# Kernel optimization log

Hardware: AMD Instinct MI355X
Metric: run time of the kernel (lower is better)

Reference implementation:

```python
import jax, jax.numpy as jnp
import numpy as np

B, F, T, C = 128, 512, 60, 15  # batch, feature_size, timesteps, num_cameras
H1, H2 = 128, 64               # decoder hidden channels


def setup_inputs() -> dict:
    key = jax.random.key(0)
    ks = jax.random.split(key, 6)
    x = jax.random.normal(ks[0], (B, F, T), dtype=jnp.float32)
    cam = jax.random.randint(ks[1], (B,), 0, C)
    # per-camera (expert) decoder params
    W1 = jax.random.normal(ks[2], (C, F, H1, 3, 4), dtype=jnp.float32) * 0.02  # ConvT3d F->128, k=(1,3,4)
    b1 = jnp.zeros((C, H1), dtype=jnp.float32)
    W2 = jax.random.normal(ks[3], (C, H1, H2, 3, 4), dtype=jnp.float32) * 0.02  # ConvT3d 128->64, k=s=(1,3,4)
    b2 = jnp.zeros((C, H2), dtype=jnp.float32)
    W3 = jax.random.normal(ks[4], (C, H2), dtype=jnp.float32) * 0.02            # Conv3d 64->1, k=1
    b3 = jnp.zeros((C,), dtype=jnp.float32)
    return {"x": x, "cam": cam, "W1": W1, "b1": b1, "W2": W2, "b2": b2, "W3": W3, "b3": b3}


def reference(x, cam, W1, b1, W2, b2, W3, b3):
    # MoE-style dispatch: gather each sample's camera-expert weights.
    # Layer 1: transposed conv from 1x1 -> 3x4 is a pure linear map over features.
    h1 = jnp.einsum('bft,bfopq->btopq', x, W1[cam]) + b1[cam][:, None, :, None, None]
    h1 = jax.nn.relu(h1)                                # (B,T,128,3,4)
    # Layer 2: stride == kernel => non-overlapping transposed conv, out[3p+r,4q+s].
    h2 = jnp.einsum('btipq,biors->btoprqs', h1, W2[cam])  # (B,T,64,3,3,4,4)
    h2 = h2.reshape(B, T, H2, 9, 16) + b2[cam][:, None, :, None, None]
    h2 = jax.nn.relu(h2)                                # (B,T,64,9,16)
    # Layer 3: 1x1x1 conv to a single channel, then squeeze + sigmoid.
    out = jnp.einsum('btohw,bo->bthw', h2, W3[cam]) + b3[cam][:, None, None, None]
    return jax.nn.sigmoid(out)                           # (B,T,9,16)
```

## Files before the change

kernel.cpp:

```cpp
#include <hip/hip_runtime.h>
#include <hip/hip_bf16.h>
#include <cstdint>

#define B_  128
#define F_  512
#define T_  60
#define C_  15
#define H1_ 128
#define H2_ 64

typedef short short8_t __attribute__((ext_vector_type(8)));
typedef float f32x4    __attribute__((ext_vector_type(4)));

static __device__ __forceinline__ unsigned short f2bf(float f) {
    union { float f; uint32_t u; } v; v.f = f;
    uint32_t r = v.u + 0x7FFF + ((v.u >> 16) & 1);
    return (unsigned short)(r >> 16);
}

static __device__ __forceinline__ void async_cp16(const unsigned short* g, unsigned short* l) {
    __builtin_amdgcn_global_load_lds(
        (const __attribute__((address_space(1))) unsigned int*)g,
        (__attribute__((address_space(3))) unsigned int*)l, 16, 0, 0);
}

__global__ __launch_bounds__(256) void prep_all(
    const float* __restrict__ x, const float* __restrict__ W2,
    const float* __restrict__ W1, const int* __restrict__ cam,
    unsigned short* __restrict__ xTs, unsigned short* __restrict__ W2f,
    unsigned short* __restrict__ W1s, int* __restrict__ ord)
{
    __shared__ float sm[12288];
    const int blk = blockIdx.x, tid = threadIdx.x;

    if (blk < 512) {
        float (*xs)[61] = (float(*)[61])sm;
        const int f0 = (blk & 3) * 128, b = blk >> 2;
        #pragma unroll
        for (int it = 0; it < 32; ++it) {
            int idx = tid + it * 256;
            int fl = idx >> 6, t = idx & 63;
            if (t < T_) xs[fl][t] = x[((size_t)b * F_ + f0 + fl) * T_ + t];
        }
        __syncthreads();
        #pragma unroll
        for (int it = 0; it < 8; ++it) {
            int idx = tid + it * 256;
            int t = idx >> 5, f4 = (idx & 31) * 4;
            ushort4 o;
            o.x = (t < T_) ? f2bf(xs[f4 + 0][t]) : 0;
            o.y = (t < T_) ? f2bf(xs[f4 + 1][t]) : 0;
            o.z = (t < T_) ? f2bf(xs[f4 + 2][t]) : 0;
            o.w = (t < T_) ? f2bf(xs[f4 + 3][t]) : 0;
            const int f = f0 + f4;
            const int kc = f >> 6, within = f & 63;
            const int cc = (within >> 3) ^ (t & 7), half = (within >> 2) & 1;
            *(ushort4*)(xTs + (size_t)b * 32768 + kc * 4096 + t * 64 + cc * 8 + half * 4) = o;
        }
    } else if (blk < 632) {
        float (*ls)[384] = (float(*)[384])sm;
        const int id = blk - 512;
        const int i0 = (id & 3) * 32, o0 = ((id >> 2) & 1) * 32, c = id >> 3;
        #pragma unroll
        for (int it = 0; it < 12; ++it) {
            int idx = tid + it * 256;
            int il = idx / 96, r = idx - il * 96;
            float4 v = *(const float4*)(W2 + ((size_t)(c * H1_ + i0 + il)) * (H2_ * 12)
                                           + (size_t)o0 * 12 + r * 4);
            *(float4*)&ls[il][r * 4] = v;
        }
        __syncthreads();
        const int o_l = tid >> 3, i_l = (tid & 7) * 4;
        const int o  = o0 + o_l;
        const int nt = o >> 4, l15 = o & 15;
        const int lane = l15 + 16 * ((i_l >> 3) & 3);
        const int kk  = i0 >> 5;
        const int pos = i_l & 7;
        #pragma unroll
        for (int rs = 0; rs < 12; ++rs) {
            ushort4 v;
            v.x = f2bf(ls[i_l + 0][o_l * 12 + rs]);
            v.y = f2bf(ls[i_l + 1][o_l * 12 + rs]);
            v.z = f2bf(ls[i_l + 2][o_l * 12 + rs]);
            v.w = f2bf(ls[i_l + 3][o_l * 12 + rs]);
            *(ushort4*)(W2f + ((size_t)(c * 12 + rs) * 16 + nt * 4 + kk) * 512
                            + lane * 8 + pos) = v;
        }
    } else if (blk == 632) {
        int* cs = (int*)sm;
        if (tid < B_) cs[tid] = cam[tid];
        __syncthreads();
        if (tid < B_) {
            const int cb = cs[tid];
            int rank = 0;
            #pragma unroll 16
            for (int j = 0; j < B_; ++j) {
                int cj = cs[j];
                rank += (cj < cb || (cj == cb && j < tid)) ? 1 : 0;
            }
            ord[rank] = tid;
        }
    } else {
        float (*ls)[384] = (float(*)[384])sm;
        const int id = blk - 633;
        const int f0 = (id & 15) * 32, i0 = ((id >> 4) & 3) * 32, c = id >> 6;
        #pragma unroll
        for (int it = 0; it < 12; ++it) {
            int idx = tid + it * 256;
            int fl = idx / 96, r = idx - fl * 96;
            float4 v = *(const float4*)(W1 + ((size_t)(c * F_ + f0 + fl)) * (H1_ * 12)
                                           + (size_t)i0 * 12 + r * 4);
            *(float4*)&ls[fl][r * 4] = v;
        }
        __syncthreads();
        const int i_l = tid >> 3, f_l = (tid & 7) * 4;
        const int i = i0 + i_l, f = f0 + f_l;
        const int kc = f >> 6, within = f & 63;
        const int cc = (within >> 3) ^ (i & 7), half = (within >> 2) & 1;
        #pragma unroll
        for (int pq = 0; pq < 12; ++pq) {
            ushort4 o;
            o.x = f2bf(ls[f_l + 0][i_l * 12 + pq]);
            o.y = f2bf(ls[f_l + 1][i_l * 12 + pq]);
            o.z = f2bf(ls[f_l + 2][i_l * 12 + pq]);
            o.w = f2bf(ls[f_l + 3][i_l * 12 + pq]);
            *(ushort4*)(W1s + (size_t)(c * 12 + pq) * 65536
                            + kc * 8192 + i * 64 + cc * 8 + half * 4) = o;
        }
    }
}

__global__ __launch_bounds__(256) void fused_all(
    const unsigned short* __restrict__ xTs, const unsigned short* __restrict__ W1s,
    const unsigned short* __restrict__ W2f, const int* __restrict__ cam,
    const int* __restrict__ ord,
    const float* __restrict__ b1, const float* __restrict__ b2,
    const float* __restrict__ W3, const float* __restrict__ b3,
    float* __restrict__ out)
{
    __shared__ __align__(16) unsigned short smem[24576];

    const int idx = blockIdx.x;
    const int swz = (idx & 7) * 192 + (idx >> 3);
    const int bpos = swz / 12, pq = swz - bpos * 12;
    const int b = ord[bpos];

    const int tid = threadIdx.x;
    const int w = tid >> 6, l = tid & 63;
    const int l15 = l & 15, g = l >> 4;
    const int c = cam[b];

    const unsigned short* xchunk = xTs + (size_t)b * 32768;
    const unsigned short* wchunk = W1s + (size_t)(c * 12 + pq) * 65536;

    #define STAGE1(kc, buf)                                                       \
        {                                                                         \
            _Pragma("unroll")                                                     \
            for (int k = 0; k < 2; ++k)                                           \
                async_cp16(xchunk + (kc) * 4096 + (w * 2 + k) * 512 + l * 8,      \
                           smem + (buf) * 12288 + (w * 2 + k) * 512 + l * 8);     \
            _Pragma("unroll")                                                     \
            for (int k = 0; k < 4; ++k)                                           \
                async_cp16(wchunk + (kc) * 8192 + (w * 4 + k) * 512 + l * 8,      \
                           smem + (buf) * 12288 + 4096 + (w * 4 + k) * 512 + l * 8); \
        }

    f32x4 acc1[4][2];
    #pragma unroll
    for (int mt = 0; mt < 4; ++mt) {
        acc1[mt][0] = (f32x4){0.f, 0.f, 0.f, 0.f};
        acc1[mt][1] = (f32x4){0.f, 0.f, 0.f, 0.f};
    }

    STAGE1(0, 0);
    STAGE1(1, 1);

    const int sxor = (l15 & 7);
    #pragma unroll
    for (int kc = 0; kc < 8; ++kc) {
        if (kc < 7) { asm volatile("s_waitcnt vmcnt(6)" ::: "memory"); }
        else        { asm volatile("s_waitcnt vmcnt(0)" ::: "memory"); }
        __builtin_amdgcn_s_barrier();
        asm volatile("" ::: "memory");

        const int base = (kc & 1) * 12288;
        #pragma unroll
        for (int kk2 = 0; kk2 < 2; ++kk2) {
            const int cc = (kk2 * 4 + g) ^ sxor;
            short8_t af[4], bf[2];
            #pragma unroll
            for (int mt = 0; mt < 4; ++mt)
                af[mt] = *(const short8_t*)(smem + base + (16 * mt + l15) * 64 + cc * 8);
            #pragma unroll
            for (int ni = 0; ni < 2; ++ni)
                bf[ni] = *(const short8_t*)(smem + base + 4096
                                            + (32 * w + 16 * ni + l15) * 64 + cc * 8);
            #pragma unroll
            for (int mt = 0; mt < 4; ++mt)
                #pragma unroll
                for (int ni = 0; ni < 2; ++ni)
                    acc1[mt][ni] = __builtin_amdgcn_mfma_f32_16x16x32_bf16(
                        af[mt], bf[ni], acc1[mt][ni], 0, 0, 0);
        }

        asm volatile("" ::: "memory");
        __builtin_amdgcn_s_barrier();
        if (kc < 6) STAGE1(kc + 2, kc & 1);
    }
    #undef STAGE1

    const unsigned short* W2base = W2f + (size_t)(c * 12 + w * 3) * 8192;
    short8_t bfr[2][4];
    #pragma unroll
    for (int kk = 0; kk < 4; ++kk)
        bfr[0][kk] = *(const short8_t*)(W2base + kk * 512 + l * 8);

    float w3v[4][4], b2v[4][4];
    #pragma unroll
    for (int nt = 0; nt < 4; ++nt)
        #pragma unroll
        for (int r = 0; r < 4; ++r) {
            w3v[nt][r] = W3[c * H2_ + nt * 16 + g * 4 + r];
            b2v[nt][r] = b2[c * H2_ + nt * 16 + g * 4 + r];
        }
    const float b3v = b3[c];
    const int p = pq >> 2, q = pq & 3;

    unsigned short* h1s = smem;
    #pragma unroll
    for (int ni = 0; ni < 2; ++ni) {
        const int i = 32 * w + 16 * ni + l15;
        const float b1v = b1[c * H1_ + i];
        #pragma unroll
        for (int mt = 0; mt < 4; ++mt)
            #pragma unroll
            for (int r = 0; r < 4; ++r) {
                float h = acc1[mt][ni][r] + b1v;
                h = h > 0.f ? h : 0.f;
                h1s[(16 * mt + 4 * g + r) * 136 + i] = f2bf(h);
            }
    }
    __syncthreads();

    short8_t a2[4][4];
    #pragma unroll
    for (int mt = 0; mt < 4; ++mt)
        #pragma unroll
        for (int kk = 0; kk < 4; ++kk)
            a2[mt][kk] = *(const short8_t*)&h1s[(16 * mt + l15) * 136 + 32 * kk + 8 * g];

    float s[4] = {0.f, 0.f, 0.f, 0.f};

    #pragma unroll
    for (int seg = 0; seg < 12; ++seg) {
        if (seg < 11) {
            const int ns = seg + 1;
            const unsigned short* nb = W2base + (ns >> 2) * 8192 + ((ns & 3) * 4) * 512;
            #pragma unroll
            for (int kk = 0; kk < 4; ++kk)
                bfr[(seg + 1) & 1][kk] = *(const short8_t*)(nb + kk * 512 + l * 8);
        }
        const int nt = seg & 3;
        #pragma unroll
        for (int mt = 0; mt < 4; ++mt) {
            f32x4 acc2 = (f32x4){0.f, 0.f, 0.f, 0.f};
            #pragma unroll
            for (int kk = 0; kk < 4; ++kk)
                acc2 = __builtin_amdgcn_mfma_f32_16x16x32_bf16(
                    bfr[seg & 1][kk], a2[mt][kk], acc2, 0, 0, 0);
            #pragma unroll
            for (int r = 0; r < 4; ++r)
                s[mt] = fmaf(w3v[nt][r], fmaxf(acc2[r] + b2v[nt][r], 0.f), s[mt]);
        }

        if (nt == 3) {
            const int rs = w * 3 + (seg >> 2);
            const int hrow = p * 3 + (rs >> 2), wcol = q * 4 + (rs & 3);
            #pragma unroll
            for (int mt = 0; mt < 4; ++mt) {
                s[mt] += __shfl_xor(s[mt], 16);
                s[mt] += __shfl_xor(s[mt], 32);
            }
            float v = (g & 1) ? ((g & 2) ? s[3] : s[1]) : ((g & 2) ? s[2] : s[0]);
            v += b3v;
            if (l < T_)
                out[(((size_t)b * T_ + l) * 9 + hrow) * 16 + wcol] =
                    1.f / (1.f + __expf(-v));
            s[0] = s[1] = s[2] = s[3] = 0.f;
        }
    }
}

__global__ __launch_bounds__(256) void fused_decoder_f32(
    const float* __restrict__ x,   const int* __restrict__ cam,
    const float* __restrict__ W1,  const float* __restrict__ b1,
    const float* __restrict__ W2,  const float* __restrict__ b2,
    const float* __restrict__ W3,  const float* __restrict__ b3,
    float* __restrict__ out)
{
    __shared__ float h1s[T_ * H1_];
    __shared__ float stage[8192];

    const int pq  = blockIdx.x;
    const int b   = blockIdx.y;
    const int p   = pq >> 2, q = pq & 3;
    const int tid = threadIdx.x;
    const int c   = cam[b];

    float* xs  = stage;
    float* w1s = stage + 2048;

    const int ig = tid & 31;
    const int tg = tid >> 5;

    float acc[8][4];
    #pragma unroll
    for (int a = 0; a < 8; ++a)
        #pragma unroll
        for (int j = 0; j < 4; ++j) acc[a][j] = 0.f;

    for (int f0 = 0; f0 < F_; f0 += 32) {
        __syncthreads();
        {
            int lane = tid & 63;
            int sub  = tid >> 6;
            if (lane < T_) {
                #pragma unroll
                for (int m = 0; m < 8; ++m) {
                    int kk = sub * 8 + m;
                    xs[kk * 64 + lane] = x[((size_t)b * F_ + f0 + kk) * T_ + lane];
                }
            }
        }
        for (int e = tid; e < 32 * H1_; e += 256) {
            int kk = e >> 7, i = e & 127;
            w1s[e] = W1[(((size_t)c * F_ + f0 + kk) * H1_ + i) * 12 + pq];
        }
        __syncthreads();
        #pragma unroll 8
        for (int kk = 0; kk < 32; ++kk) {
            float4 bv = *(const float4*)&w1s[kk * 128 + ig * 4];
            float4 a0 = *(const float4*)&xs[kk * 64 + tg * 8];
            float4 a1 = *(const float4*)&xs[kk * 64 + tg * 8 + 4];
            float at[8] = {a0.x, a0.y, a0.z, a0.w, a1.x, a1.y, a1.z, a1.w};
            #pragma unroll
            for (int tt = 0; tt < 8; ++tt) {
                acc[tt][0] = fmaf(at[tt], bv.x, acc[tt][0]);
                acc[tt][1] = fmaf(at[tt], bv.y, acc[tt][1]);
                acc[tt][2] = fmaf(at[tt], bv.z, acc[tt][2]);
                acc[tt][3] = fmaf(at[tt], bv.w, acc[tt][3]);
            }
        }
    }
    {
        float4 b1v = *(const float4*)&b1[c * H1_ + ig * 4];
        #pragma unroll
        for (int tt = 0; tt < 8; ++tt) {
            int t = tg * 8 + tt;
            if (t < T_) {
                float4 hv;
                hv.x = fmaxf(acc[tt][0] + b1v.x, 0.f);
                hv.y = fmaxf(acc[tt][1] + b1v.y, 0.f);
                hv.z = fmaxf(acc[tt][2] + b1v.z, 0.f);
                hv.w = fmaxf(acc[tt][3] + b1v.w, 0.f);
                *(float4*)&h1s[t * H1_ + ig * 4] = hv;
            }
        }
    }

    const int lane = tid & 63;
    const int wv   = tid >> 6;
    const float w3v = W3[c * H2_ + lane];
    const float b2v = b2[c * H2_ + lane];
    const float b3v = b3[c];
    float* w2s = stage;

    for (int rs = 0; rs < 12; ++rs) {
        __syncthreads();
        for (int e = tid; e < H1_ * H2_; e += 256) {
            int i = e >> 6, o = e & 63;
            w2s[e] = W2[(((size_t)c * H1_ + i) * H2_ + o) * 12 + rs];
        }
        __syncthreads();

        float acc2[15];
        #pragma unroll
        for (int j = 0; j < 15; ++j) acc2[j] = 0.f;

        for (int i = 0; i < H1_; i += 4) {
            float wa = w2s[(i + 0) * 64 + lane];
            float wb = w2s[(i + 1) * 64 + lane];
            float wc = w2s[(i + 2) * 64 + lane];
            float wd = w2s[(i + 3) * 64 + lane];
            #pragma unroll
            for (int j = 0; j < 15; ++j) {
                float4 h = *(const float4*)&h1s[(wv * 15 + j) * H1_ + i];
                acc2[j] = fmaf(h.x, wa, acc2[j]);
                acc2[j] = fmaf(h.y, wb, acc2[j]);
                acc2[j] = fmaf(h.z, wc, acc2[j]);
                acc2[j] = fmaf(h.w, wd, acc2[j]);
            }
        }

        const int r = rs >> 2, s = rs & 3;
        const int hrow = p * 3 + r, wcol = q * 4 + s;
        #pragma unroll
        for (int j = 0; j < 15; ++j) {
            float y = w3v * fmaxf(acc2[j] + b2v, 0.f);
            #pragma unroll
            for (int m = 32; m > 0; m >>= 1) y += __shfl_xor(y, m, 64);
            if (lane == j) {
                int t = wv * 15 + j;
                float v = y + b3v;
                out[(((size_t)b * T_ + t) * 9 + hrow) * 16 + wcol] = 1.f / (1.f + __expf(-v));
            }
        }
    }
}

extern "C" void kernel_launch(void* const* d_in, const int* in_sizes, int n_in,
                              void* d_out, int out_size, void* d_ws, size_t ws_size,
                              hipStream_t stream) {
    const float* x   = (const float*)d_in[0];
    const int*   cam = (const int*)  d_in[1];
    const float* W1  = (const float*)d_in[2];
    const float* b1  = (const float*)d_in[3];
    const float* W2  = (const float*)d_in[4];
    const float* b2  = (const float*)d_in[5];
    const float* W3  = (const float*)d_in[6];
    const float* b3  = (const float*)d_in[7];
    float* outp = (float*)d_out;

    const size_t n_xT  = (size_t)B_ * 32768;
    const size_t n_w1s = (size_t)C_ * 12 * 65536;
    const size_t n_w2f = (size_t)C_ * 12 * 16 * 512;
    const size_t needed = (n_xT + n_w1s + n_w2f) * sizeof(unsigned short)
                        + B_ * sizeof(int);

    if (d_ws != nullptr && ws_size >= needed) {
        unsigned short* xTs = (unsigned short*)d_ws;
        unsigned short* W1p = xTs + n_xT;
        unsigned short* W2p = W1p + n_w1s;
        int* ord = (int*)(W2p + n_w2f);
        prep_all<<<1593, 256, 0, stream>>>(x, W2, W1, cam, xTs, W2p, W1p, ord);
        fused_all<<<dim3(12 * B_), 256, 0, stream>>>(
            xTs, W1p, W2p, cam, ord, b1, b2, W3, b3, outp);
    } else {
        fused_decoder_f32<<<dim3(12, B_), 256, 0, stream>>>(
            x, cam, W1, b1, W2, b2, W3, b3, outp);
    }
}
```

Baseline: 60.58 us.

## Pair same-camera samples per block to share expert weight tiles

The prep kernel now groups samples with the same camera into chunks of up to two, and the fused kernel processes one chunk per block. The W1 expert tile is loaded once and used for two samples, doubling the M dimension of the first GEMM. Layer 2 runs once per sample and reuses the same W2 stream. This roughly halves W1 traffic and block count, at the cost of a larger LDS footprint (64KB), twice as many accumulator registers, fewer blocks, and duplicate work when a camera has an odd number of samples.

```diff
diff --git a/kernel.cpp b/kernel.cpp
--- a/kernel.cpp
+++ b/kernel.cpp
@@ -28,7 +28,8 @@
     const float* __restrict__ x, const float* __restrict__ W2,
     const float* __restrict__ W1, const int* __restrict__ cam,
     unsigned short* __restrict__ xTs, unsigned short* __restrict__ W2f,
-    unsigned short* __restrict__ W1s, int* __restrict__ ord)
+    unsigned short* __restrict__ W1s, int* __restrict__ chunks,
+    int* __restrict__ nchp)
 {
     __shared__ float sm[12288];
     const int blk = blockIdx.x, tid = threadIdx.x;
@@ -87,7 +88,8 @@
                             + lane * 8 + pos) = v;
         }
     } else if (blk == 632) {
-        int* cs = (int*)sm;
+        int* cs  = (int*)sm;
+        int* ods = cs + 128;
         if (tid < B_) cs[tid] = cam[tid];
         __syncthreads();
         if (tid < B_) {
@@ -98,7 +100,20 @@
                 int cj = cs[j];
                 rank += (cj < cb || (cj == cb && j < tid)) ? 1 : 0;
             }
-            ord[rank] = tid;
+            ods[rank] = tid;
+        }
+        __syncthreads();
+        if (tid == 0) {
+            int k = 0, j = 0;
+            while (j < B_) {
+                int b0 = ods[j], bn;
+                if (j + 1 < B_ && cs[ods[j + 1]] == cs[b0]) { bn = ods[j + 1]; j += 2; }
+                else { bn = b0; j += 1; }
+                chunks[2 * k]     = b0;
+                chunks[2 * k + 1] = bn;
+                ++k;
+            }
+            nchp[0] = k;
         }
     } else {
         float (*ls)[384] = (float(*)[384])sm;
@@ -133,41 +148,47 @@
 __global__ __launch_bounds__(256) void fused_all(
     const unsigned short* __restrict__ xTs, const unsigned short* __restrict__ W1s,
     const unsigned short* __restrict__ W2f, const int* __restrict__ cam,
-    const int* __restrict__ ord,
+    const int* __restrict__ chunks, const int* __restrict__ nchp,
     const float* __restrict__ b1, const float* __restrict__ b2,
     const float* __restrict__ W3, const float* __restrict__ b3,
     float* __restrict__ out)
 {
-    __shared__ __align__(16) unsigned short smem[24576];
+    __shared__ __align__(16) unsigned short smem[32768];
 
     const int idx = blockIdx.x;
-    const int swz = (idx & 7) * 192 + (idx >> 3);
-    const int bpos = swz / 12, pq = swz - bpos * 12;
-    const int b = ord[bpos];
+    const int swz = (idx & 7) * 108 + (idx >> 3);
+    const int chunk = swz / 12, pq = swz - chunk * 12;
+    if (chunk >= nchp[0]) return;
+    const int bA = chunks[2 * chunk], bB = chunks[2 * chunk + 1];
 
     const int tid = threadIdx.x;
     const int w = tid >> 6, l = tid & 63;
     const int l15 = l & 15, g = l >> 4;
-    const int c = cam[b];
-
-    const unsigned short* xchunk = xTs + (size_t)b * 32768;
+    const int c = cam[bA];
+
+    const unsigned short* xcA = xTs + (size_t)bA * 32768;
+    const unsigned short* xcB = xTs + (size_t)bB * 32768;
     const unsigned short* wchunk = W1s + (size_t)(c * 12 + pq) * 65536;
 
     #define STAGE1(kc, buf)                                                       \
         {                                                                         \
             _Pragma("unroll")                                                     \
             for (int k = 0; k < 2; ++k)                                           \
-                async_cp16(xchunk + (kc) * 4096 + (w * 2 + k) * 512 + l * 8,      \
-                           smem + (buf) * 12288 + (w * 2 + k) * 512 + l * 8);     \
+                async_cp16(xcA + (kc) * 4096 + (w * 2 + k) * 512 + l * 8,         \
+                           smem + (buf) * 16384 + (w * 2 + k) * 512 + l * 8);     \
+            _Pragma("unroll")                                                     \
+            for (int k = 0; k < 2; ++k)                                           \
+                async_cp16(xcB + (kc) * 4096 + (w * 2 + k) * 512 + l * 8,         \
+                           smem + (buf) * 16384 + 4096 + (w * 2 + k) * 512 + l * 8); \
             _Pragma("unroll")                                                     \
             for (int k = 0; k < 4; ++k)                                           \
                 async_cp16(wchunk + (kc) * 8192 + (w * 4 + k) * 512 + l * 8,      \
-                           smem + (buf) * 12288 + 4096 + (w * 4 + k) * 512 + l * 8); \
-        }
-
-    f32x4 acc1[4][2];
-    #pragma unroll
-    for (int mt = 0; mt < 4; ++mt) {
+                           smem + (buf) * 16384 + 8192 + (w * 4 + k) * 512 + l * 8); \
+        }
+
+    f32x4 acc1[8][2];
+    #pragma unroll
+    for (int mt = 0; mt < 8; ++mt) {
         acc1[mt][0] = (f32x4){0.f, 0.f, 0.f, 0.f};
         acc1[mt][1] = (f32x4){0.f, 0.f, 0.f, 0.f};
     }
@@ -178,25 +199,29 @@
     const int sxor = (l15 & 7);
     #pragma unroll
     for (int kc = 0; kc < 8; ++kc) {
-        if (kc < 7) { asm volatile("s_waitcnt vmcnt(6)" ::: "memory"); }
+        if (kc < 7) { asm volatile("s_waitcnt vmcnt(8)" ::: "memory"); }
         else        { asm volatile("s_waitcnt vmcnt(0)" ::: "memory"); }
         __builtin_amdgcn_s_barrier();
         asm volatile("" ::: "memory");
 
-        const int base = (kc & 1) * 12288;
+        const int base = (kc & 1) * 16384;
         #pragma unroll
         for (int kk2 = 0; kk2 < 2; ++kk2) {
             const int cc = (kk2 * 4 + g) ^ sxor;
-            short8_t af[4], bf[2];
+            short8_t af[8], bf[2];
             #pragma unroll
             for (int mt = 0; mt < 4; ++mt)
                 af[mt] = *(const short8_t*)(smem + base + (16 * mt + l15) * 64 + cc * 8);
             #pragma unroll
+            for (int mt = 0; mt < 4; ++mt)
+                af[4 + mt] = *(const short8_t*)(smem + base + 4096
+                                                + (16 * mt + l15) * 64 + cc * 8);
+            #pragma unroll
             for (int ni = 0; ni < 2; ++ni)
-                bf[ni] = *(const short8_t*)(smem + base + 4096
+                bf[ni] = *(const short8_t*)(smem + base + 8192
                                             + (32 * w + 16 * ni + l15) * 64 + cc * 8);
             #pragma unroll
-            for (int mt = 0; mt < 4; ++mt)
+            for (int mt = 0; mt < 8; ++mt)
                 #pragma unroll
                 for (int ni = 0; ni < 2; ++ni)
                     acc1[mt][ni] = __builtin_amdgcn_mfma_f32_16x16x32_bf16(
@@ -226,67 +251,81 @@
     const float b3v = b3[c];
     const int p = pq >> 2, q = pq & 3;
 
-    unsigned short* h1s = smem;
     #pragma unroll
     for (int ni = 0; ni < 2; ++ni) {
         const int i = 32 * w + 16 * ni + l15;
         const float b1v = b1[c * H1_ + i];
         #pragma unroll
-        for (int mt = 0; mt < 4; ++mt)
+        for (int mt = 0; mt < 8; ++mt) {
+            unsigned short* h1s = smem + (mt >> 2) * 16384;
+            const int mtl = mt & 3;
             #pragma unroll
             for (int r = 0; r < 4; ++r) {
                 float h = acc1[mt][ni][r] + b1v;
                 h = h > 0.f ? h : 0.f;
-                h1s[(16 * mt + 4 * g + r) * 136 + i] = f2bf(h);
-            }
+                h1s[(16 * mtl + 4 * g + r) * 136 + i] = f2bf(h);
+            }
+        }
     }
     __syncthreads();
 
-    short8_t a2[4][4];
-    #pragma unroll
-    for (int mt = 0; mt < 4; ++mt)
-        #pragma unroll
-        for (int kk = 0; kk < 4; ++kk)
-            a2[mt][kk] = *(const short8_t*)&h1s[(16 * mt + l15) * 136 + 32 * kk + 8 * g];
-
-    float s[4] = {0.f, 0.f, 0.f, 0.f};
-
-    #pragma unroll
-    for (int seg = 0; seg < 12; ++seg) {
-        if (seg < 11) {
-            const int ns = seg + 1;
-            const unsigned short* nb = W2base + (ns >> 2) * 8192 + ((ns & 3) * 4) * 512;
+    #pragma unroll
+    for (int smp = 0; smp < 2; ++smp) {
+        const unsigned short* h1s = smem + smp * 16384;
+        const int bb = smp ? bB : bA;
+
+        short8_t a2[4][4];
+        #pragma unroll
+        for (int mt = 0; mt < 4; ++mt)
             #pragma unroll
             for (int kk = 0; kk < 4; ++kk)
-                bfr[(seg + 1) & 1][kk] = *(const short8_t*)(nb + kk * 512 + l * 8);
-        }
-        const int nt = seg & 3;
-        #pragma unroll
-        for (int mt = 0; mt < 4; ++mt) {
-            f32x4 acc2 = (f32x4){0.f, 0.f, 0.f, 0.f};
+                a2[mt][kk] = *(const short8_t*)&h1s[(16 * mt + l15) * 136 + 32 * kk + 8 * g];
+
+        if (smp == 1) {
             #pragma unroll
             for (int kk = 0; kk < 4; ++kk)
-                acc2 = __builtin_amdgcn_mfma_f32_16x16x32_bf16(
-                    bfr[seg & 1][kk], a2[mt][kk], acc2, 0, 0, 0);
-            #pragma unroll
-            for (int r = 0; r < 4; ++r)
-                s[mt] = fmaf(w3v[nt][r], fmaxf(acc2[r] + b2v[nt][r], 0.f), s[mt]);
-        }
-
-        if (nt == 3) {
-            const int rs = w * 3 + (seg >> 2);
-            const int hrow = p * 3 + (rs >> 2), wcol = q * 4 + (rs & 3);
+                bfr[0][kk] = *(const short8_t*)(W2base + kk * 512 + l * 8);
+        }
+
+        float s[4] = {0.f, 0.f, 0.f, 0.f};
+
+        #pragma unroll
+        for (int seg = 0; seg < 12; ++seg) {
+            if (seg < 11) {
+                const int ns = seg + 1;
+                const unsigned short* nb = W2base + (ns >> 2) * 8192 + ((ns & 3) * 4) * 512;
+                #pragma unroll
+                for (int kk = 0; kk < 4; ++kk)
+                    bfr[(seg + 1) & 1][kk] = *(const short8_t*)(nb + kk * 512 + l * 8);
+            }
+            const int nt = seg & 3;
             #pragma unroll
             for (int mt = 0; mt < 4; ++mt) {
-                s[mt] += __shfl_xor(s[mt], 16);
-                s[mt] += __shfl_xor(s[mt], 32);
-            }
-            float v = (g & 1) ? ((g & 2) ? s[3] : s[1]) : ((g & 2) ? s[2] : s[0]);
-            v += b3v;
-            if (l < T_)
-                out[(((size_t)b * T_ + l) * 9 + hrow) * 16 + wcol] =
-                    1.f / (1.f + __expf(-v));
-            s[0] = s[1] = s[2] = s[3] = 0.f;
+                f32x4 acc2 = (f32x4){0.f, 0.f, 0.f, 0.f};
+                #pragma unroll
+                for (int kk = 0; kk < 4; ++kk)
+                    acc2 = __builtin_amdgcn_mfma_f32_16x16x32_bf16(
+                        bfr[seg & 1][kk], a2[mt][kk], acc2, 0, 0, 0);
+                #pragma unroll
+                for (int r = 0; r < 4; ++r)
+                    s[mt] = fmaf(w3v[nt][r], fmaxf(acc2[r] + b2v[nt][r], 0.f), s[mt]);
+            }
+
+            if (nt == 3) {
+                const int rs = w * 3 + (seg >> 2);
+                const int hrow = p * 3 + (rs >> 2), wcol = q * 4 + (rs & 3);
+                #pragma unroll
+                for (int mt = 0; mt < 4; ++mt) {
+                    s[mt] += __shfl_xor(s[mt], 16);
+                    s[mt] += __shfl_xor(s[mt], 32);
+                }
+                float v = (g & 1) ? ((g & 2) ? s[3] : s[1]) : ((g & 2) ? s[2] : s[0]);
+                v += b3v;
+                if (l < T_)
+                    out[(((size_t)bb * T_ + l) * 9 + hrow) * 16 + wcol] =
+                        1.f / (1.f + __expf(-v));
+                s[0] = s[1] = s[2] = s[3] = 0.f;
+            }
         }
     }
 }
@@ -435,16 +474,17 @@
     const size_t n_w1s = (size_t)C_ * 12 * 65536;
     const size_t n_w2f = (size_t)C_ * 12 * 16 * 512;
     const size_t needed = (n_xT + n_w1s + n_w2f) * sizeof(unsigned short)
-                        + B_ * sizeof(int);
+                        + (144 + 1) * sizeof(int);
 
     if (d_ws != nullptr && ws_size >= needed) {
         unsigned short* xTs = (unsigned short*)d_ws;
         unsigned short* W1p = xTs + n_xT;
         unsigned short* W2p = W1p + n_w1s;
-        int* ord = (int*)(W2p + n_w2f);
-        prep_all<<<1593, 256, 0, stream>>>(x, W2, W1, cam, xTs, W2p, W1p, ord);
-        fused_all<<<dim3(12 * B_), 256, 0, stream>>>(
-            xTs, W1p, W2p, cam, ord, b1, b2, W3, b3, outp);
+        int* chunks = (int*)(W2p + n_w2f);
+        int* nchp   = chunks + 144;
+        prep_all<<<1593, 256, 0, stream>>>(x, W2, W1, cam, xTs, W2p, W1p, chunks, nchp);
+        fused_all<<<dim3(864), 256, 0, stream>>>(
+            xTs, W1p, W2p, cam, chunks, nchp, b1, b2, W3, b3, outp);
     } else {
         fused_decoder_f32<<<dim3(12, B_), 256, 0, stream>>>(
             x, cam, W1, b1, W2, b2, W3, b3, outp);
```

Result: slower. 79.27 us (+30.9%).
